# Performance work log

Hardware: AMD Instinct MI355X
Metric: run time of the kernel (lower is better)

The kernel has to match this reference:

```python
import jax, jax.numpy as jnp
import numpy as np

TOPK = 9
NUM_CLASSES = 80
NUM_ANCHORS_LIST = [6400, 1600, 400]  # strides 8/16/32 on 640x640
EPS = 1e-9


def bbox_center(b):
    return (b[..., :2] + b[..., 2:]) * 0.5


def pairwise_iou(b1, b2):
    # b1: (B,n,4), b2: (B or 1, L, 4) -> (B,n,L)
    lt = jnp.maximum(b1[:, :, None, :2], b2[:, None, :, :2])
    rb = jnp.minimum(b1[:, :, None, 2:], b2[:, None, :, 2:])
    wh = jnp.clip(rb - lt, 0.0)
    inter = wh[..., 0] * wh[..., 1]
    a1 = (b1[..., 2] - b1[..., 0]) * (b1[..., 3] - b1[..., 1])
    a2 = (b2[..., 2] - b2[..., 0]) * (b2[..., 3] - b2[..., 1])
    union = a1[:, :, None] + a2[:, None, :] - inter + EPS
    return inter / union


def atss_forward(anchor_bboxes, gt_labels, gt_bboxes, pad_gt_mask, pred_bboxes, bg_index):
    B, n = gt_bboxes.shape[:2]
    L = anchor_bboxes.shape[0]
    dt = gt_bboxes.dtype

    ious = pairwise_iou(gt_bboxes, anchor_bboxes[None])              # (B,n,L)
    gt_c = bbox_center(gt_bboxes)                                    # (B,n,2)
    a_c = bbox_center(anchor_bboxes)                                 # (L,2)
    dists = jnp.linalg.norm(gt_c[:, :, None] - a_c[None, None], axis=-1)  # (B,n,L)

    pad_bool = pad_gt_mask[..., 0] > 0                               # (B,n)
    bi = jnp.arange(B)[:, None, None]
    gi = jnp.arange(n)[None, :, None]
    is_in_topk_parts, topk_idx_parts = [], []
    start = 0
    for nl in NUM_ANCHORS_LIST:  # fixed small set of pyramid levels
        d = jax.lax.dynamic_slice_in_dim(dists, start, nl, axis=-1)
        _, idx = jax.lax.top_k(-d, TOPK)                             # k smallest distances
        topk_idx_parts.append(idx + start)
        idx0 = jnp.where(pad_bool[..., None], idx, 0)
        # scatter-count instead of materializing (B,n,TOPK,nl) one-hot
        cnt = jnp.zeros((B, n, nl), dt).at[bi, gi, idx0].add(1.0)
        is_in_topk_parts.append(jnp.where(cnt > 1, 0.0, cnt))
        start += nl
    is_in_topk = jnp.concatenate(is_in_topk_parts, -1)               # (B,n,L)
    topk_idxs = jnp.concatenate(topk_idx_parts, -1)                  # (B,n,3*TOPK)

    iou_cand = ious * is_in_topk
    thr_samp = jnp.take_along_axis(iou_cand, topk_idxs, axis=-1)     # (B,n,27)
    thr = thr_samp.mean(-1, keepdims=True) + jnp.std(thr_samp, axis=-1, keepdims=True, ddof=1)
    is_in_topk = jnp.where(iou_cand > thr, is_in_topk, 0.0)

    # anchor centers strictly inside gt boxes
    lt = a_c[None, None] - gt_bboxes[:, :, None, :2]
    rb = gt_bboxes[:, :, None, 2:] - a_c[None, None]
    is_in_gts = (jnp.minimum(lt, rb).min(-1) > EPS).astype(dt)       # (B,n,L)

    mask_positive = is_in_topk * is_in_gts * pad_gt_mask             # (B,n,L)
    mps = mask_positive.sum(1)                                       # (B,L)

    # anchors matched to multiple gts -> keep highest-iou gt (no-op if none)
    multi = mps[:, None, :] > 1
    max_idx = jnp.argmax(ious, axis=1)                               # (B,L)
    is_max_iou = (jnp.arange(n)[None, :, None] == max_idx[:, None, :]).astype(dt)
    mask_positive = jnp.where(multi, is_max_iou, mask_positive)
    mps = mask_positive.sum(1)

    agi = jnp.argmax(mask_positive, axis=1)                          # (B,L)
    labels = jnp.take_along_axis(gt_labels[..., 0], agi, axis=1)
    labels = jnp.where(mps > 0, labels, bg_index).astype(jnp.int32)
    bboxes = jnp.take_along_axis(gt_bboxes, agi[..., None], axis=1)  # (B,L,4)

    scores = jax.nn.one_hot(labels, NUM_CLASSES + 1, dtype=jnp.float32)
    keep = np.array([i for i in range(NUM_CLASSES + 1) if i != bg_index])
    scores = scores[..., keep]                                       # (B,L,C)

    ious_pred = pairwise_iou(gt_bboxes, pred_bboxes) * mask_positive
    scores = scores * ious_pred.max(1)[..., None]
    return labels, bboxes, scores


def setup_inputs() -> dict:
    key = jax.random.key(0)
    ks = jax.random.split(key, 6)
    B, n = 32, 128
    anchors = []
    for fs, stride in [(80, 8), (40, 16), (20, 32)]:
        xs = (jnp.arange(fs, dtype=jnp.float32) + 0.5) * stride
        cy, cx = jnp.meshgrid(xs, xs, indexing='ij')
        c = jnp.stack([cx.ravel(), cy.ravel()], -1)
        half = 2.5 * stride
        anchors.append(jnp.concatenate([c - half, c + half], -1))
    anchor_bboxes = jnp.concatenate(anchors, 0)                      # (8400,4)
    L = anchor_bboxes.shape[0]
    cxy = jax.random.uniform(ks[0], (B, n, 2), minval=0.0, maxval=640.0)
    wh = jax.random.uniform(ks[1], (B, n, 2), minval=10.0, maxval=300.0)
    gt_bboxes = jnp.concatenate([cxy - wh / 2, cxy + wh / 2], -1)
    gt_labels = jax.random.randint(ks[2], (B, n, 1), 0, 80).astype(jnp.int32)
    nvalid = jax.random.randint(ks[3], (B, 1), 16, n + 1)
    pad_gt_mask = (jnp.arange(n)[None] < nvalid).astype(jnp.float32)[..., None]
    a_c = bbox_center(anchor_bboxes)
    pc = a_c[None] + 8.0 * jax.random.normal(ks[4], (B, L, 2))
    pwh = jax.random.uniform(ks[5], (B, L, 2), minval=20.0, maxval=200.0)
    pred_bboxes = jnp.concatenate([pc - pwh / 2, pc + pwh / 2], -1)
    return {"anchor_bboxes": anchor_bboxes, "gt_labels": gt_labels,
            "gt_bboxes": gt_bboxes, "pad_gt_mask": pad_gt_mask,
            "pred_bboxes": pred_bboxes, "bg_index": 80}


def reference(anchor_bboxes, gt_labels, gt_bboxes, pad_gt_mask, pred_bboxes, bg_index):
    return atss_forward(anchor_bboxes, gt_labels, gt_bboxes, pad_gt_mask, pred_bboxes, bg_index)
```

## Files before the change

### kernel.cpp

```cpp
#include <hip/hip_runtime.h>
#include <cstdint>

#define NB   32
#define NGT  128
#define NL   8400
#define TK   9
#define NC   80
#define FEPS 1e-9f

typedef unsigned long long u64;

__device__ __forceinline__ float iou_box(float ax0, float ay0, float ax1, float ay1,
                                         float bx0, float by0, float bx1, float by1) {
#pragma clang fp contract(off)
    float lx = fmaxf(ax0, bx0), ly = fmaxf(ay0, by0);
    float rx = fminf(ax1, bx1), ry = fminf(ay1, by1);
    float w = fmaxf(rx - lx, 0.f), h = fmaxf(ry - ly, 0.f);
    float inter = w * h;
    float a1 = (ax1 - ax0) * (ay1 - ay0);
    float a2 = (bx1 - bx0) * (by1 - by0);
    float uni = a1 + a2 - inter + FEPS;
    return inter / uni;
}

__device__ __forceinline__ void anchor_box(int a, float& x0, float& y0, float& x1, float& y1) {
    int fs, rem; float s;
    if (a < 6400)      { fs = 80; s = 8.f;  rem = a; }
    else if (a < 8000) { fs = 40; s = 16.f; rem = a - 6400; }
    else               { fs = 20; s = 32.f; rem = a - 8000; }
    int iy = rem / fs, ix = rem - iy * fs;
    float cx = ((float)ix + 0.5f) * s, cy = ((float)iy + 0.5f) * s, h = 2.5f * s;
    x0 = cx - h; y0 = cy - h; x1 = cx + h; y1 = cy + h;
}

__global__ void __launch_bounds__(192)
atss_topk_kernel(const float* __restrict__ gtb, const float* __restrict__ padm,
                 int* __restrict__ cand) {
#pragma clang fp contract(off)
    __shared__ float siou[64][27];
    __shared__ int   sidx[64][27];

    const int tid = threadIdx.x;
    const int gl  = tid & 63;
    const int lv  = tid >> 6;
    const int p   = blockIdx.x * 64 + gl;

    const float4 gb = ((const float4*)gtb)[p];
    const float gx0 = gb.x, gy0 = gb.y, gx1 = gb.z, gy1 = gb.w;
    const float gcx = (gx0 + gx1) * 0.5f, gcy = (gy0 + gy1) * 0.5f;

    {
        const int   fs   = (lv == 0) ? 80 : (lv == 1 ? 40 : 20);
        const float s    = (lv == 0) ? 8.f : (lv == 1 ? 16.f : 32.f);
        const int   base = (lv == 0) ? 0 : (lv == 1 ? 6400 : 8000);

        const int fx = (int)floorf(gcx / s - 0.5f);
        const int fy = (int)floorf(gcy / s - 0.5f);
        const int lox = min(max(fx - 4, 0), fs - 10);
        const int loy = min(max(fy - 4, 0), fs - 10);

        u64 sk[TK];
#pragma unroll
        for (int j = 0; j < TK; ++j) sk[j] = ~0ULL;

        for (int r = 0; r < 10; ++r) {
            const int iy = loy + r;
            const float ay = ((float)iy + 0.5f) * s;
            const float dy = gcy - ay;
            const float dy2 = dy * dy;
            const int rowbase = base + iy * fs + lox;
#pragma unroll
            for (int c = 0; c < 10; ++c) {
                const float ax = ((float)(lox + c) + 0.5f) * s;
                const float dx = gcx - ax;
                const float d = sqrtf(dx * dx + dy2);
                u64 nk = ((u64)__float_as_uint(d) << 32) | (unsigned int)(rowbase + c);
#pragma unroll
                for (int j = 0; j < TK; ++j) {
                    const u64 sj = sk[j];
                    const u64 mn = (nk < sj) ? nk : sj;
                    nk = (nk < sj) ? sj : nk;
                    sk[j] = mn;
                }
            }
        }

#pragma unroll
        for (int j = 0; j < TK; ++j) {
            const int id = (int)(unsigned int)(sk[j] & 0xffffffffu);
            float ax0, ay0, ax1, ay1;
            anchor_box(id, ax0, ay0, ax1, ay1);
            siou[gl][lv * TK + j] = iou_box(gx0, gy0, gx1, gy1, ax0, ay0, ax1, ay1);
            sidx[gl][lv * TK + j] = id;
        }
    }
    __syncthreads();

    if (tid < 64) {
        int* cp = cand + (size_t)p * 27;
        if (padm[p] <= 0.f) {
#pragma unroll
            for (int k = 0; k < 27; ++k) cp[k] = -1;
            return;
        }
        float sum = 0.f;
#pragma unroll
        for (int k = 0; k < 27; ++k) sum += siou[gl][k];
        const float mean = sum / 27.f;
        float d2 = 0.f;
#pragma unroll
        for (int k = 0; k < 27; ++k) {
            const float e = siou[gl][k] - mean;
            d2 += e * e;
        }
        const float thr = mean + sqrtf(d2 / 26.f);

#pragma unroll
        for (int k = 0; k < 27; ++k) {
            const int id = sidx[gl][k];
            int keep = -1;
            if (siou[gl][k] > thr) {
                float ax0, ay0, ax1, ay1;
                anchor_box(id, ax0, ay0, ax1, ay1);
                const float acx = (ax0 + ax1) * 0.5f, acy = (ay0 + ay1) * 0.5f;
                const float l = acx - gx0, t = acy - gy0, r = gx1 - acx, bo = gy1 - acy;
                const float mn = fminf(fminf(l, t), fminf(r, bo));
                if (mn > FEPS) keep = id;
            }
            cp[k] = keep;
        }
    }
}

__global__ void __launch_bounds__(256)
atss_assign_kernel(const int* __restrict__ gtl, const float* __restrict__ gtb,
                   const float* __restrict__ pred, const int* __restrict__ bgp,
                   const int* __restrict__ cand, float* __restrict__ out) {
#pragma clang fp contract(off)
    __shared__ unsigned int smask[256][4];
    __shared__ float4 sgt[NGT];
    __shared__ int    slbl[NGT];
    __shared__ int    s_lab[256];
    __shared__ float  s_iou[256];

    const int tid = threadIdx.x;
    const int b = blockIdx.y;
    const int a0 = blockIdx.x * 256;
    const int nA = min(256, NL - a0);

    smask[tid][0] = 0; smask[tid][1] = 0; smask[tid][2] = 0; smask[tid][3] = 0;
    if (tid < NGT) {
        sgt[tid]  = ((const float4*)gtb)[b * NGT + tid];
        slbl[tid] = gtl[b * NGT + tid];
    }
    __syncthreads();

    const int* cb = cand + (size_t)b * NGT * 27;
    for (int f = tid; f < NGT * 27; f += 256) {
        const int id = cb[f];
        const int la = id - a0;
        if (la >= 0 && la < nA) {
            const int g = f / 27;
            atomicOr(&smask[la][g >> 5], 1u << (g & 31));
        }
    }
    __syncthreads();

    int lbl = 0, pos = 0;
    float ioup = 0.f;
    const int a = a0 + tid;
    if (a < NL) {
        const int t = b * NL + a;
        const unsigned int m0 = smask[tid][0], m1 = smask[tid][1];
        const unsigned int m2 = smask[tid][2], m3 = smask[tid][3];
        const int mps = __popc(m0) + __popc(m1) + __popc(m2) + __popc(m3);
        int agi = 0;
        if (mps > 1) {
            float ax0, ay0, ax1, ay1;
            anchor_box(a, ax0, ay0, ax1, ay1);
            float best = -1.f;
            for (int gg = 0; gg < NGT; ++gg) {
                const float4 q = sgt[gg];
                const float v = iou_box(q.x, q.y, q.z, q.w, ax0, ay0, ax1, ay1);
                if (v > best) { best = v; agi = gg; }
            }
            pos = 1;
        } else if (mps == 1) {
            if (m0)      agi = __ffs(m0) - 1;
            else if (m1) agi = 32 + __ffs(m1) - 1;
            else if (m2) agi = 64 + __ffs(m2) - 1;
            else         agi = 96 + __ffs(m3) - 1;
            pos = 1;
        }
        const int bgi = *bgp;
        lbl = pos ? slbl[agi] : bgi;
        out[t] = (float)lbl;

        const float4 q = sgt[agi];
        ((float4*)(out + (size_t)NB * NL))[t] = q;

        if (pos) {
            const float4 pb = ((const float4*)pred)[t];
            ioup = iou_box(q.x, q.y, q.z, q.w, pb.x, pb.y, pb.z, pb.w);
        }
    }
    s_lab[tid] = pos ? lbl : -1;
    s_iou[tid] = ioup;
    __syncthreads();

    float4* osb = (float4*)(out + (size_t)NB * NL * 5 + ((size_t)b * NL + a0) * NC);
    const int total4 = nA * (NC / 4);
    for (int e = tid; e < total4; e += 256) {
        const int ai = e / (NC / 4);
        const int c0 = (e - ai * (NC / 4)) * 4;
        const int lb = s_lab[ai];
        const float v = s_iou[ai];
        float4 o;
        o.x = (c0     == lb) ? v : 0.f;
        o.y = (c0 + 1 == lb) ? v : 0.f;
        o.z = (c0 + 2 == lb) ? v : 0.f;
        o.w = (c0 + 3 == lb) ? v : 0.f;
        osb[e] = o;
    }
}

extern "C" void kernel_launch(void* const* d_in, const int* in_sizes, int n_in,
                              void* d_out, int out_size, void* d_ws, size_t ws_size,
                              hipStream_t stream) {
    const int*   gtl  = (const int*)d_in[1];
    const float* gtb  = (const float*)d_in[2];
    const float* padm = (const float*)d_in[3];
    const float* pred = (const float*)d_in[4];
    const int*   bgp  = (const int*)d_in[5];

    int* cand = (int*)d_ws;

    atss_topk_kernel<<<NB * NGT / 64, 192, 0, stream>>>(gtb, padm, cand);

    dim3 grid((NL + 255) / 256, NB);
    atss_assign_kernel<<<grid, 256, 0, stream>>>(gtl, gtb, pred, bgp, cand, (float*)d_out);
}
```

Measured before the change: 151.5 us.

## Fuse topk and assign kernels into one cooperative kernel with grid sync

Merges the two launches into a single cooperative kernel of 256 persistent blocks. The first 64 blocks compute per-GT top-k candidates, a grid-wide sync follows, and then all blocks loop over the batch×anchor tiles to do assignment. This removes one kernel launch and the gap between kernels. In exchange it adds grid-barrier overhead, and the first phase runs on only a quarter of the blocks while the rest wait.

```diff
diff --git a/kernel.cpp b/kernel.cpp
--- a/kernel.cpp
+++ b/kernel.cpp
@@ -1,5 +1,8 @@
 #include <hip/hip_runtime.h>
+#include <hip/hip_cooperative_groups.h>
 #include <cstdint>
+
+namespace cg = cooperative_groups;
 
 #define NB   32
 #define NGT  128
@@ -7,6 +10,8 @@
 #define TK   9
 #define NC   80
 #define FEPS 1e-9f
+#define NTILE 33
+#define GRID  256
 
 typedef unsigned long long u64;
 
@@ -33,23 +38,32 @@
     x0 = cx - h; y0 = cy - h; x1 = cx + h; y1 = cy + h;
 }
 
-__global__ void __launch_bounds__(192)
-atss_topk_kernel(const float* __restrict__ gtb, const float* __restrict__ padm,
-                 int* __restrict__ cand) {
+__global__ void __launch_bounds__(256)
+atss_fused_kernel(const int* __restrict__ gtl, const float* __restrict__ gtb,
+                  const float* __restrict__ padm, const float* __restrict__ pred,
+                  const int* __restrict__ bgp, int* __restrict__ cand,
+                  float* __restrict__ out) {
 #pragma clang fp contract(off)
     __shared__ float siou[64][27];
     __shared__ int   sidx[64][27];
-
+    __shared__ unsigned int smask[256][4];
+    __shared__ float4 sgt[NGT];
+    __shared__ int    slbl[NGT];
+    __shared__ int    s_lab[256];
+    __shared__ float  s_iou[256];
+
+    cg::grid_group grid = cg::this_grid();
     const int tid = threadIdx.x;
-    const int gl  = tid & 63;
-    const int lv  = tid >> 6;
-    const int p   = blockIdx.x * 64 + gl;
-
-    const float4 gb = ((const float4*)gtb)[p];
-    const float gx0 = gb.x, gy0 = gb.y, gx1 = gb.z, gy1 = gb.w;
-    const float gcx = (gx0 + gx1) * 0.5f, gcy = (gy0 + gy1) * 0.5f;
-
-    {
+
+    if (blockIdx.x < 64 && tid < 192) {
+        const int gl = tid & 63;
+        const int lv = tid >> 6;
+        const int p  = blockIdx.x * 64 + gl;
+
+        const float4 gb = ((const float4*)gtb)[p];
+        const float gx0 = gb.x, gy0 = gb.y, gx1 = gb.z, gy1 = gb.w;
+        const float gcx = (gx0 + gx1) * 0.5f, gcy = (gy0 + gy1) * 0.5f;
+
         const int   fs   = (lv == 0) ? 80 : (lv == 1 ? 40 : 20);
         const float s    = (lv == 0) ? 8.f : (lv == 1 ? 16.f : 32.f);
         const int   base = (lv == 0) ? 0 : (lv == 1 ? 6400 : 8000);
@@ -84,7 +98,6 @@
                 }
             }
         }
-
 #pragma unroll
         for (int j = 0; j < TK; ++j) {
             const int id = (int)(unsigned int)(sk[j] & 0xffffffffu);
@@ -95,132 +108,125 @@
         }
     }
     __syncthreads();
-
-    if (tid < 64) {
+    if (blockIdx.x < 64 && tid < 64) {
+        const int p = blockIdx.x * 64 + tid;
         int* cp = cand + (size_t)p * 27;
         if (padm[p] <= 0.f) {
 #pragma unroll
             for (int k = 0; k < 27; ++k) cp[k] = -1;
-            return;
-        }
-        float sum = 0.f;
-#pragma unroll
-        for (int k = 0; k < 27; ++k) sum += siou[gl][k];
-        const float mean = sum / 27.f;
-        float d2 = 0.f;
-#pragma unroll
-        for (int k = 0; k < 27; ++k) {
-            const float e = siou[gl][k] - mean;
-            d2 += e * e;
-        }
-        const float thr = mean + sqrtf(d2 / 26.f);
-
-#pragma unroll
-        for (int k = 0; k < 27; ++k) {
-            const int id = sidx[gl][k];
-            int keep = -1;
-            if (siou[gl][k] > thr) {
+        } else {
+            const float4 gb = ((const float4*)gtb)[p];
+            const float gx0 = gb.x, gy0 = gb.y, gx1 = gb.z, gy1 = gb.w;
+            float sum = 0.f;
+#pragma unroll
+            for (int k = 0; k < 27; ++k) sum += siou[tid][k];
+            const float mean = sum / 27.f;
+            float d2 = 0.f;
+#pragma unroll
+            for (int k = 0; k < 27; ++k) {
+                const float e = siou[tid][k] - mean;
+                d2 += e * e;
+            }
+            const float thr = mean + sqrtf(d2 / 26.f);
+#pragma unroll
+            for (int k = 0; k < 27; ++k) {
+                const int id = sidx[tid][k];
+                int keep = -1;
+                if (siou[tid][k] > thr) {
+                    float ax0, ay0, ax1, ay1;
+                    anchor_box(id, ax0, ay0, ax1, ay1);
+                    const float acx = (ax0 + ax1) * 0.5f, acy = (ay0 + ay1) * 0.5f;
+                    const float l = acx - gx0, t = acy - gy0, r = gx1 - acx, bo = gy1 - acy;
+                    const float mn = fminf(fminf(l, t), fminf(r, bo));
+                    if (mn > FEPS) keep = id;
+                }
+                cp[k] = keep;
+            }
+        }
+    }
+
+    grid.sync();
+
+    const int bgi = *bgp;
+    for (int vb = blockIdx.x; vb < NB * NTILE; vb += GRID) {
+        const int b = vb / NTILE;
+        const int a0 = (vb - b * NTILE) * 256;
+        const int nA = min(256, NL - a0);
+
+        smask[tid][0] = 0; smask[tid][1] = 0; smask[tid][2] = 0; smask[tid][3] = 0;
+        if (tid < NGT) {
+            sgt[tid]  = ((const float4*)gtb)[b * NGT + tid];
+            slbl[tid] = gtl[b * NGT + tid];
+        }
+        __syncthreads();
+
+        const int* cb = cand + (size_t)b * NGT * 27;
+        for (int f = tid; f < NGT * 27; f += 256) {
+            const int id = cb[f];
+            const int la = id - a0;
+            if (la >= 0 && la < nA) {
+                const int g = f / 27;
+                atomicOr(&smask[la][g >> 5], 1u << (g & 31));
+            }
+        }
+        __syncthreads();
+
+        int lbl = 0, pos = 0;
+        float ioup = 0.f;
+        const int a = a0 + tid;
+        if (a < NL) {
+            const int t = b * NL + a;
+            const unsigned int m0 = smask[tid][0], m1 = smask[tid][1];
+            const unsigned int m2 = smask[tid][2], m3 = smask[tid][3];
+            const int mps = __popc(m0) + __popc(m1) + __popc(m2) + __popc(m3);
+            int agi = 0;
+            if (mps > 1) {
                 float ax0, ay0, ax1, ay1;
-                anchor_box(id, ax0, ay0, ax1, ay1);
-                const float acx = (ax0 + ax1) * 0.5f, acy = (ay0 + ay1) * 0.5f;
-                const float l = acx - gx0, t = acy - gy0, r = gx1 - acx, bo = gy1 - acy;
-                const float mn = fminf(fminf(l, t), fminf(r, bo));
-                if (mn > FEPS) keep = id;
-            }
-            cp[k] = keep;
-        }
-    }
-}
-
-__global__ void __launch_bounds__(256)
-atss_assign_kernel(const int* __restrict__ gtl, const float* __restrict__ gtb,
-                   const float* __restrict__ pred, const int* __restrict__ bgp,
-                   const int* __restrict__ cand, float* __restrict__ out) {
-#pragma clang fp contract(off)
-    __shared__ unsigned int smask[256][4];
-    __shared__ float4 sgt[NGT];
-    __shared__ int    slbl[NGT];
-    __shared__ int    s_lab[256];
-    __shared__ float  s_iou[256];
-
-    const int tid = threadIdx.x;
-    const int b = blockIdx.y;
-    const int a0 = blockIdx.x * 256;
-    const int nA = min(256, NL - a0);
-
-    smask[tid][0] = 0; smask[tid][1] = 0; smask[tid][2] = 0; smask[tid][3] = 0;
-    if (tid < NGT) {
-        sgt[tid]  = ((const float4*)gtb)[b * NGT + tid];
-        slbl[tid] = gtl[b * NGT + tid];
-    }
-    __syncthreads();
-
-    const int* cb = cand + (size_t)b * NGT * 27;
-    for (int f = tid; f < NGT * 27; f += 256) {
-        const int id = cb[f];
-        const int la = id - a0;
-        if (la >= 0 && la < nA) {
-            const int g = f / 27;
-            atomicOr(&smask[la][g >> 5], 1u << (g & 31));
-        }
-    }
-    __syncthreads();
-
-    int lbl = 0, pos = 0;
-    float ioup = 0.f;
-    const int a = a0 + tid;
-    if (a < NL) {
-        const int t = b * NL + a;
-        const unsigned int m0 = smask[tid][0], m1 = smask[tid][1];
-        const unsigned int m2 = smask[tid][2], m3 = smask[tid][3];
-        const int mps = __popc(m0) + __popc(m1) + __popc(m2) + __popc(m3);
-        int agi = 0;
-        if (mps > 1) {
-            float ax0, ay0, ax1, ay1;
-            anchor_box(a, ax0, ay0, ax1, ay1);
-            float best = -1.f;
-            for (int gg = 0; gg < NGT; ++gg) {
-                const float4 q = sgt[gg];
-                const float v = iou_box(q.x, q.y, q.z, q.w, ax0, ay0, ax1, ay1);
-                if (v > best) { best = v; agi = gg; }
-            }
-            pos = 1;
-        } else if (mps == 1) {
-            if (m0)      agi = __ffs(m0) - 1;
-            else if (m1) agi = 32 + __ffs(m1) - 1;
-            else if (m2) agi = 64 + __ffs(m2) - 1;
-            else         agi = 96 + __ffs(m3) - 1;
-            pos = 1;
-        }
-        const int bgi = *bgp;
-        lbl = pos ? slbl[agi] : bgi;
-        out[t] = (float)lbl;
-
-        const float4 q = sgt[agi];
-        ((float4*)(out + (size_t)NB * NL))[t] = q;
-
-        if (pos) {
-            const float4 pb = ((const float4*)pred)[t];
-            ioup = iou_box(q.x, q.y, q.z, q.w, pb.x, pb.y, pb.z, pb.w);
-        }
-    }
-    s_lab[tid] = pos ? lbl : -1;
-    s_iou[tid] = ioup;
-    __syncthreads();
-
-    float4* osb = (float4*)(out + (size_t)NB * NL * 5 + ((size_t)b * NL + a0) * NC);
-    const int total4 = nA * (NC / 4);
-    for (int e = tid; e < total4; e += 256) {
-        const int ai = e / (NC / 4);
-        const int c0 = (e - ai * (NC / 4)) * 4;
-        const int lb = s_lab[ai];
-        const float v = s_iou[ai];
-        float4 o;
-        o.x = (c0     == lb) ? v : 0.f;
-        o.y = (c0 + 1 == lb) ? v : 0.f;
-        o.z = (c0 + 2 == lb) ? v : 0.f;
-        o.w = (c0 + 3 == lb) ? v : 0.f;
-        osb[e] = o;
+                anchor_box(a, ax0, ay0, ax1, ay1);
+                float best = -1.f;
+                for (int gg = 0; gg < NGT; ++gg) {
+                    const float4 q = sgt[gg];
+                    const float v = iou_box(q.x, q.y, q.z, q.w, ax0, ay0, ax1, ay1);
+                    if (v > best) { best = v; agi = gg; }
+                }
+                pos = 1;
+            } else if (mps == 1) {
+                if (m0)      agi = __ffs(m0) - 1;
+                else if (m1) agi = 32 + __ffs(m1) - 1;
+                else if (m2) agi = 64 + __ffs(m2) - 1;
+                else         agi = 96 + __ffs(m3) - 1;
+                pos = 1;
+            }
+            lbl = pos ? slbl[agi] : bgi;
+            out[t] = (float)lbl;
+
+            const float4 q = sgt[agi];
+            ((float4*)(out + (size_t)NB * NL))[t] = q;
+
+            if (pos) {
+                const float4 pb = ((const float4*)pred)[t];
+                ioup = iou_box(q.x, q.y, q.z, q.w, pb.x, pb.y, pb.z, pb.w);
+            }
+        }
+        s_lab[tid] = pos ? lbl : -1;
+        s_iou[tid] = ioup;
+        __syncthreads();
+
+        float4* osb = (float4*)(out + (size_t)NB * NL * 5 + ((size_t)b * NL + a0) * NC);
+        const int total4 = nA * (NC / 4);
+        for (int e = tid; e < total4; e += 256) {
+            const int ai = e / (NC / 4);
+            const int c0 = (e - ai * (NC / 4)) * 4;
+            const int lb = s_lab[ai];
+            const float v = s_iou[ai];
+            float4 o;
+            o.x = (c0     == lb) ? v : 0.f;
+            o.y = (c0 + 1 == lb) ? v : 0.f;
+            o.z = (c0 + 2 == lb) ? v : 0.f;
+            o.w = (c0 + 3 == lb) ? v : 0.f;
+            osb[e] = o;
+        }
+        __syncthreads();
     }
 }
 
@@ -232,11 +238,11 @@
     const float* padm = (const float*)d_in[3];
     const float* pred = (const float*)d_in[4];
     const int*   bgp  = (const int*)d_in[5];
-
-    int* cand = (int*)d_ws;
-
-    atss_topk_kernel<<<NB * NGT / 64, 192, 0, stream>>>(gtb, padm, cand);
-
-    dim3 grid((NL + 255) / 256, NB);
-    atss_assign_kernel<<<grid, 256, 0, stream>>>(gtl, gtb, pred, bgp, cand, (float*)d_out);
-}
+    int*         cand = (int*)d_ws;
+    float*       out  = (float*)d_out;
+
+    void* args[] = {(void*)&gtl, (void*)&gtb, (void*)&padm, (void*)&pred,
+                    (void*)&bgp, (void*)&cand, (void*)&out};
+    (void)hipLaunchCooperativeKernel((const void*)atss_fused_kernel,
+                                     dim3(GRID), dim3(256), args, 0, stream);
+}
```

Result: slower. 209.1 us (+38.0%).
